# Kernel tuning notes

Measured on AMD Instinct MI355X. Metric: run time of the kernel, lower is better.

## Reference

```python
import jax, jax.numpy as jnp
import numpy as np

B, N = 32, 2048
W_POINT, W_CHAMFER, W_STRUCT = 1.0, 5.0, 2.0
BIG = 1e10  # finite sentinel for masked-out distances
EPS = 1e-12


def setup_inputs() -> dict:
    key = jax.random.key(0)
    k1, k2, k3, k4, k5 = jax.random.split(key, 5)
    pred_xy = jax.random.normal(k1, (B, N, 2), dtype=jnp.float32)
    pred_v = jax.random.bernoulli(k2, 0.95, (B, N, 1)).astype(jnp.float32)
    tgt_xy = jax.random.normal(k3, (B, N, 2), dtype=jnp.float32)
    tgt_v = jax.random.bernoulli(k4, 0.95, (B, N, 1)).astype(jnp.float32)
    pred = jnp.concatenate([pred_xy, pred_v], axis=-1)
    target = jnp.concatenate([tgt_xy, tgt_v], axis=-1)
    skeleton_mask = jax.random.bernoulli(k5, 0.1, (B, N, 2)).astype(jnp.float32)
    return {"pred": pred, "target": target, "skeleton_mask": skeleton_mask}


def _skeleton_loss(pred, target, skeleton_mask):
    dt = pred.dtype
    tv = target[..., 2] == 1.0              # [B,N] valid target points
    vm = tv[..., None].astype(dt)           # [B,N,1]

    # masked MSE over coordinates (mean over ALL B*N*2 elements, as torch.mean)
    coord_err = (pred[..., :2] - target[..., :2]) * vm
    loss_point = jnp.mean(coord_err ** 2)

    # chamfer distance with validity masking (vectorized over batch)
    pv = pred[..., 2] == 1.0                # [B,N] valid pred points
    P, T = pred[..., :2], target[..., :2]
    d2 = (jnp.sum(P * P, -1)[:, :, None] + jnp.sum(T * T, -1)[:, None, :]
          - 2.0 * jnp.einsum('bnd,bmd->bnm', P, T))       # [B,Np,Nt]
    d = jnp.sqrt(jnp.maximum(d2, EPS))
    pvf = pv.astype(dt)
    tvf = tv.astype(dt)
    # pred -> target: min over valid target cols, mean over valid pred rows
    min_p = jnp.min(jnp.where(tv[:, None, :], d, BIG), axis=2)   # [B,Np]
    cnt_p = jnp.sum(pvf, axis=1)
    mean_p = jnp.sum(min_p * pvf, axis=1) / jnp.maximum(cnt_p, 1.0)
    # target -> pred
    min_t = jnp.min(jnp.where(pv[:, None, :], jnp.swapaxes(d, 1, 2), BIG), axis=2)
    cnt_t = jnp.sum(tvf, axis=1)
    mean_t = jnp.sum(min_t * tvf, axis=1) / jnp.maximum(cnt_t, 1.0)
    both = (cnt_p > 0) & (cnt_t > 0)
    chamfer_b = jnp.where(both, (mean_p + mean_t) * 0.5, 0.0)
    loss_chamfer = jnp.sum(chamfer_b) / B

    # structural point loss
    structure_mask = jnp.clip(skeleton_mask[..., 0] + skeleton_mask[..., 1], 0.0, 1.0)[..., None]
    total_mask = structure_mask * vm
    struct_err = (pred[..., :2] - target[..., :2]) * total_mask
    loss_structure = jnp.where(jnp.sum(total_mask) > 0, jnp.mean(struct_err ** 2), 0.0)

    total = W_POINT * loss_point + W_CHAMFER * loss_chamfer + W_STRUCT * loss_structure
    vis = jnp.zeros((), dtype=dt)
    # [skeleton_total_loss, skeleton_point_loss, skeleton_visibility_loss, skeleton_shape_loss]
    return jnp.stack([total, loss_point, vis, loss_chamfer])


def reference(pred, target, skeleton_mask):
    return _skeleton_loss(pred, target, skeleton_mask)
```

## Files before the change

### kernel.cpp

```cpp
#include <hip/hip_runtime.h>
#include <math.h>

#define BB 32
#define NN 2048
#define TB 256
#define QT 4
#define QPB (QT * TB)
#define QB (NN / QPB)
#define K2_QB (NN / TB)


__device__ __forceinline__ float wred(float v) {
#pragma unroll
    for (int o = 32; o > 0; o >>= 1) v += __shfl_down(v, o, 64);
    return v;
}

__global__ __launch_bounds__(256) void k1_chamfer(
    const float* __restrict__ pred, const float* __restrict__ tgt,
    float* __restrict__ part, int R)
{
    __shared__ float4 sref[NN];

    const int tid  = threadIdx.x;
    const int b    = blockIdx.y;
    const int role = blockIdx.z & 1;
    const int rc   = blockIdx.z >> 1;
    const int M    = NN / R;

    const float* q = role ? tgt : pred;
    const float* r = role ? pred : tgt;
    const float* rb = r + ((size_t)b * NN + (size_t)rc * M) * 3;

    for (int m = tid; m < M; m += TB) {
        float rx = rb[3 * m + 0];
        float ry = rb[3 * m + 1];
        float rv = rb[3 * m + 2];
        if (rv != 1.0f) { rx = 1.0e9f; ry = 1.0e9f; }
        sref[m] = make_float4(-2.0f * rx, -2.0f * ry, fmaf(rx, rx, ry * ry), 0.0f);
    }
    __syncthreads();

    const float* qb_ = q + (size_t)b * NN * 3;
    const int q0 = blockIdx.x * QPB + tid;

    float px[QT], py[QT], mn[QT];
#pragma unroll
    for (int j = 0; j < QT; j++) {
        int qi = q0 + j * TB;
        px[j] = qb_[3 * qi + 0];
        py[j] = qb_[3 * qi + 1];
        mn[j] = 3.4e38f;
    }

#pragma unroll 4
    for (int m = 0; m < M; m++) {
        float4 t = sref[m];
#pragma unroll
        for (int j = 0; j < QT; j++) {
            float s = fmaf(px[j], t.x, fmaf(py[j], t.y, t.z));
            mn[j] = fminf(mn[j], s);
        }
    }

#pragma unroll
    for (int j = 0; j < QT; j++) {
        int qi = q0 + j * TB;
        float qn = fmaf(px[j], px[j], py[j] * py[j]);
        part[((size_t)(role * BB + b) * NN + qi) * (size_t)R + rc] = qn + mn[j];
    }
}

__global__ __launch_bounds__(256) void k2_combine(
    const float* __restrict__ pred, const float* __restrict__ tgt,
    const float* __restrict__ smask, const float* __restrict__ part,
    float* __restrict__ bsum, int R)
{
    __shared__ float sred[5 * 4];
    const int tid  = threadIdx.x;
    const int b    = blockIdx.y;
    const int role = blockIdx.z;
    const int qi   = blockIdx.x * TB + tid;

    const float* pbase = part + ((size_t)(role * BB + b) * NN + qi) * (size_t)R;
    float m = 3.4e38f;
    for (int rr = 0; rr < R; rr++) m = fminf(m, pbase[rr]);

    const float* qp = (role ? tgt : pred) + ((size_t)b * NN + qi) * 3;
    float qvf = (qp[2] == 1.0f) ? 1.0f : 0.0f;
    float contrib = sqrtf(fmaxf(m, 1e-12f)) * qvf;

    float pt = 0.0f, st = 0.0f, mk = 0.0f;
    if (role == 0) {
        float px = qp[0], py = qp[1];
        const float* tp = tgt + ((size_t)b * NN + qi) * 3;
        float vm = (tp[2] == 1.0f) ? 1.0f : 0.0f;
        float dx = px - tp[0], dy = py - tp[1];
        float e2 = fmaf(dx, dx, dy * dy);
        float s0 = smask[((size_t)b * NN + qi) * 2 + 0];
        float s1 = smask[((size_t)b * NN + qi) * 2 + 1];
        float tm = fminf(fmaxf(s0 + s1, 0.0f), 1.0f) * vm;
        pt = e2 * vm;
        st = e2 * tm;
        mk = tm;
    }

    float v[5] = {contrib, qvf, pt, st, mk};
    const int wave = tid >> 6, lane = tid & 63;
#pragma unroll
    for (int i = 0; i < 5; i++) {
        float rv = wred(v[i]);
        if (lane == 0) sred[i * 4 + wave] = rv;
    }
    __syncthreads();
    if (tid < 5) {
        int i = tid;
        float s = sred[i * 4 + 0] + sred[i * 4 + 1] + sred[i * 4 + 2] + sred[i * 4 + 3];
        int slot = (role * BB + b) * K2_QB + blockIdx.x;
        bsum[i * (2 * BB * K2_QB) + slot] = s;
    }
}

__global__ __launch_bounds__(64) void k3_final(
    const float* __restrict__ bsum, float* __restrict__ out)
{
    const int lane = threadIdx.x;
    const int S = 2 * BB * K2_QB;

    float ch = 0.0f;
    if (lane < BB) {
        float sp = 0, cp = 0, stt = 0, ct = 0;
#pragma unroll
        for (int x = 0; x < K2_QB; x++) {
            sp += bsum[0 * S + (0 * BB + lane) * K2_QB + x];
            cp += bsum[1 * S + (0 * BB + lane) * K2_QB + x];
            stt += bsum[0 * S + (1 * BB + lane) * K2_QB + x];
            ct += bsum[1 * S + (1 * BB + lane) * K2_QB + x];
        }
        float mp = sp / fmaxf(cp, 1.0f);
        float mt = stt / fmaxf(ct, 1.0f);
        ch = (cp > 0.0f && ct > 0.0f) ? 0.5f * (mp + mt) : 0.0f;
    }
    ch = wred(ch);

    float spt = 0, sst = 0, smk = 0;
    for (int i = lane; i < S; i += 64) {
        spt += bsum[2 * S + i];
        sst += bsum[3 * S + i];
        smk += bsum[4 * S + i];
    }
    spt = wred(spt); sst = wred(sst); smk = wred(smk);

    if (lane == 0) {
        float loss_chamfer = ch / (float)BB;
        const float denom = (float)BB * (float)NN * 2.0f;
        float loss_point = spt / denom;
        float loss_struct = (smk > 0.0f) ? sst / denom : 0.0f;
        out[0] = loss_point + 5.0f * loss_chamfer + 2.0f * loss_struct;
        out[1] = loss_point;
        out[2] = 0.0f;
        out[3] = loss_chamfer;
    }
}

extern "C" void kernel_launch(void* const* d_in, const int* in_sizes, int n_in,
                              void* d_out, int out_size, void* d_ws, size_t ws_size,
                              hipStream_t stream)
{
    const float* pred  = (const float*)d_in[0];
    const float* tgt   = (const float*)d_in[1];
    const float* smask = (const float*)d_in[2];
    float* out = (float*)d_out;
    float* ws  = (float*)d_ws;

    int R = 8;
    while (R > 1) {
        size_t need = ((size_t)2 * BB * NN * R + 5 * 2 * BB * K2_QB) * sizeof(float);
        if (need <= ws_size) break;
        R >>= 1;
    }
    float* part = ws;
    float* bsum = ws + (size_t)2 * BB * NN * R;

    k1_chamfer<<<dim3(QB, BB, 2 * R), TB, 0, stream>>>(pred, tgt, part, R);
    k2_combine<<<dim3(K2_QB, BB, 2), TB, 0, stream>>>(pred, tgt, smask, part, bsum, R);
    k3_final<<<1, 64, 0, stream>>>(bsum, out);
}
```

Baseline: 82.76 us.

## Retile chamfer kernel: 8 queries per thread, SoA shared ref, coalesced partials

Each block now covers all 2048 queries of a batch against one of 8 fixed reference chunks, with 8 query points per thread instead of 4. Reference data moves to three structure-of-arrays shared buffers read as float4, so one LDS load serves four reference points. Partial minima are stored chunk-major so the combine kernel reads them coalesced. This removes the workspace-size fallback and halves the grid to 512 blocks, which may lower occupancy, and it assumes the workspace is large enough for 8 chunks.

```diff
diff --git a/kernel.cpp b/kernel.cpp
--- a/kernel.cpp
+++ b/kernel.cpp
@@ -4,9 +4,9 @@
 #define BB 32
 #define NN 2048
 #define TB 256
-#define QT 4
-#define QPB (QT * TB)
-#define QB (NN / QPB)
+#define QT 8
+#define RCH 8
+#define MCH (NN / RCH)
 #define K2_QB (NN / TB)
 
 
@@ -18,63 +18,67 @@
 
 __global__ __launch_bounds__(256) void k1_chamfer(
     const float* __restrict__ pred, const float* __restrict__ tgt,
-    float* __restrict__ part, int R)
+    float* __restrict__ part)
 {
-    __shared__ float4 sref[NN];
+    __shared__ float sa[MCH], sb[MCH], sc[MCH];
 
     const int tid  = threadIdx.x;
     const int b    = blockIdx.y;
     const int role = blockIdx.z & 1;
     const int rc   = blockIdx.z >> 1;
-    const int M    = NN / R;
 
     const float* q = role ? tgt : pred;
     const float* r = role ? pred : tgt;
-    const float* rb = r + ((size_t)b * NN + (size_t)rc * M) * 3;
+    const float* rb = r + ((size_t)b * NN + (size_t)rc * MCH) * 3;
 
-    for (int m = tid; m < M; m += TB) {
-        float rx = rb[3 * m + 0];
-        float ry = rb[3 * m + 1];
-        float rv = rb[3 * m + 2];
+    {
+        float rx = rb[3 * tid + 0];
+        float ry = rb[3 * tid + 1];
+        float rv = rb[3 * tid + 2];
         if (rv != 1.0f) { rx = 1.0e9f; ry = 1.0e9f; }
-        sref[m] = make_float4(-2.0f * rx, -2.0f * ry, fmaf(rx, rx, ry * ry), 0.0f);
+        sa[tid] = -2.0f * rx;
+        sb[tid] = -2.0f * ry;
+        sc[tid] = fmaf(rx, rx, ry * ry);
     }
     __syncthreads();
 
     const float* qb_ = q + (size_t)b * NN * 3;
-    const int q0 = blockIdx.x * QPB + tid;
-
     float px[QT], py[QT], mn[QT];
 #pragma unroll
     for (int j = 0; j < QT; j++) {
-        int qi = q0 + j * TB;
+        int qi = tid + j * TB;
         px[j] = qb_[3 * qi + 0];
         py[j] = qb_[3 * qi + 1];
         mn[j] = 3.4e38f;
     }
 
-#pragma unroll 4
-    for (int m = 0; m < M; m++) {
-        float4 t = sref[m];
+#pragma unroll 2
+    for (int m = 0; m < MCH; m += 4) {
+        float4 a4 = *(const float4*)&sa[m];
+        float4 b4 = *(const float4*)&sb[m];
+        float4 c4 = *(const float4*)&sc[m];
 #pragma unroll
         for (int j = 0; j < QT; j++) {
-            float s = fmaf(px[j], t.x, fmaf(py[j], t.y, t.z));
-            mn[j] = fminf(mn[j], s);
+            float s0 = fmaf(px[j], a4.x, fmaf(py[j], b4.x, c4.x));
+            float s1 = fmaf(px[j], a4.y, fmaf(py[j], b4.y, c4.y));
+            float s2 = fmaf(px[j], a4.z, fmaf(py[j], b4.z, c4.z));
+            float s3 = fmaf(px[j], a4.w, fmaf(py[j], b4.w, c4.w));
+            mn[j] = fminf(fminf(fminf(fminf(s0, s1), s2), s3), mn[j]);
         }
     }
 
 #pragma unroll
     for (int j = 0; j < QT; j++) {
-        int qi = q0 + j * TB;
+        int qi = tid + j * TB;
         float qn = fmaf(px[j], px[j], py[j] * py[j]);
-        part[((size_t)(role * BB + b) * NN + qi) * (size_t)R + rc] = qn + mn[j];
+        part[((size_t)rc * (2 * BB) + role * BB + b) * NN + qi] = qn + mn[j];
     }
 }
 
 __global__ __launch_bounds__(256) void k2_combine(
     const float* __restrict__ pred, const float* __restrict__ tgt,
     const float* __restrict__ smask, const float* __restrict__ part,
-    float* __restrict__ bsum, int R)
+    float* __restrict__ bsum)
 {
     __shared__ float sred[5 * 4];
     const int tid  = threadIdx.x;
@@ -82,9 +86,10 @@
     const int role = blockIdx.z;
     const int qi   = blockIdx.x * TB + tid;
 
-    const float* pbase = part + ((size_t)(role * BB + b) * NN + qi) * (size_t)R;
     float m = 3.4e38f;
-    for (int rr = 0; rr < R; rr++) m = fminf(m, pbase[rr]);
+#pragma unroll
+    for (int rc = 0; rc < RCH; rc++)
+        m = fminf(m, part[((size_t)rc * (2 * BB) + role * BB + b) * NN + qi]);
 
     const float* qp = (role ? tgt : pred) + ((size_t)b * NN + qi) * 3;
     float qvf = (qp[2] == 1.0f) ? 1.0f : 0.0f;
@@ -132,10 +137,10 @@
         float sp = 0, cp = 0, stt = 0, ct = 0;
 #pragma unroll
         for (int x = 0; x < K2_QB; x++) {
-            sp += bsum[0 * S + (0 * BB + lane) * K2_QB + x];
-            cp += bsum[1 * S + (0 * BB + lane) * K2_QB + x];
+            sp  += bsum[0 * S + (0 * BB + lane) * K2_QB + x];
+            cp  += bsum[1 * S + (0 * BB + lane) * K2_QB + x];
             stt += bsum[0 * S + (1 * BB + lane) * K2_QB + x];
-            ct += bsum[1 * S + (1 * BB + lane) * K2_QB + x];
+            ct  += bsum[1 * S + (1 * BB + lane) * K2_QB + x];
         }
         float mp = sp / fmaxf(cp, 1.0f);
         float mt = stt / fmaxf(ct, 1.0f);
@@ -173,16 +178,10 @@
     float* out = (float*)d_out;
     float* ws  = (float*)d_ws;
 
-    int R = 8;
-    while (R > 1) {
-        size_t need = ((size_t)2 * BB * NN * R + 5 * 2 * BB * K2_QB) * sizeof(float);
-        if (need <= ws_size) break;
-        R >>= 1;
-    }
     float* part = ws;
-    float* bsum = ws + (size_t)2 * BB * NN * R;
+    float* bsum = ws + (size_t)RCH * 2 * BB * NN;
 
-    k1_chamfer<<<dim3(QB, BB, 2 * R), TB, 0, stream>>>(pred, tgt, part, R);
-    k2_combine<<<dim3(K2_QB, BB, 2), TB, 0, stream>>>(pred, tgt, smask, part, bsum, R);
+    k1_chamfer<<<dim3(1, BB, 2 * RCH), TB, 0, stream>>>(pred, tgt, part);
+    k2_combine<<<dim3(K2_QB, BB, 2), TB, 0, stream>>>(pred, tgt, smask, part, bsum);
     k3_final<<<1, 64, 0, stream>>>(bsum, out);
 }
```

New measurement: 81.26 us. No clear change (-1.8%).
